# Optimization experiments

Hardware: AMD Instinct MI355X
Metric: run time of the kernel (lower is better)

## Reference

```python
import jax, jax.numpy as jnp
import numpy as np

N_LAYERS = 6
N_HEADS = 16
D_MODEL = 1024
D_HEAD = D_MODEL // N_HEADS
D_FF = 4096
VOCAB = 32000
MAX_LEN = 1024
B, T = 2, 1024
NEG = -1e9
EPS = 1e-5


def layernorm(x, s, b):
    mu = jnp.mean(x, axis=-1, keepdims=True)
    var = jnp.mean(jnp.square(x - mu), axis=-1, keepdims=True)
    return (x - mu) * jax.lax.rsqrt(var + EPS) * s + b


def setup_inputs() -> dict:
    key = jax.random.key(0)
    ks = jax.random.split(key, 8)
    s = 0.02
    return {
        "idx": jax.random.randint(ks[0], (B, T), 0, VOCAB),
        "tok_emb": jax.random.normal(ks[1], (VOCAB, D_MODEL), jnp.float32) * s,
        "pos_emb": jax.random.normal(ks[2], (MAX_LEN, D_MODEL), jnp.float32) * s,
        "ln1_s": jnp.ones((N_LAYERS, D_MODEL), jnp.float32),
        "ln1_b": jnp.zeros((N_LAYERS, D_MODEL), jnp.float32),
        "qkv_w": jax.random.normal(ks[3], (N_LAYERS, D_MODEL, 3 * D_MODEL), jnp.float32) * s,
        "qkv_b": jnp.zeros((N_LAYERS, 3 * D_MODEL), jnp.float32),
        "out_w": jax.random.normal(ks[4], (N_LAYERS, D_MODEL, D_MODEL), jnp.float32) * s,
        "out_b": jnp.zeros((N_LAYERS, D_MODEL), jnp.float32),
        "ln2_s": jnp.ones((N_LAYERS, D_MODEL), jnp.float32),
        "ln2_b": jnp.zeros((N_LAYERS, D_MODEL), jnp.float32),
        "mlp_w1": jax.random.normal(ks[5], (N_LAYERS, D_MODEL, D_FF), jnp.float32) * s,
        "mlp_b1": jnp.zeros((N_LAYERS, D_FF), jnp.float32),
        "mlp_w2": jax.random.normal(ks[6], (N_LAYERS, D_FF, D_MODEL), jnp.float32) * s,
        "mlp_b2": jnp.zeros((N_LAYERS, D_MODEL), jnp.float32),
        "lnf_s": jnp.ones((D_MODEL,), jnp.float32),
        "lnf_b": jnp.zeros((D_MODEL,), jnp.float32),
        "head_w": jax.random.normal(ks[7], (D_MODEL, VOCAB), jnp.float32) * s,
    }


def reference(idx, tok_emb, pos_emb, ln1_s, ln1_b, qkv_w, qkv_b, out_w, out_b,
              ln2_s, ln2_b, mlp_w1, mlp_b1, mlp_w2, mlp_b2, lnf_s, lnf_b, head_w):
    b, t = idx.shape
    x = tok_emb[idx] + pos_emb[:t]  # [B,T,D]
    causal = jnp.tril(jnp.ones((t, t), dtype=bool))
    scale = 1.0 / np.sqrt(D_HEAD)
    for l in range(N_LAYERS):
        h = layernorm(x, ln1_s[l], ln1_b[l])
        qkv = h @ qkv_w[l] + qkv_b[l]  # [B,T,3D]
        q, k, v = jnp.split(qkv, 3, axis=-1)
        q = q.reshape(b, t, N_HEADS, D_HEAD).transpose(0, 2, 1, 3)
        k = k.reshape(b, t, N_HEADS, D_HEAD).transpose(0, 2, 1, 3)
        v = v.reshape(b, t, N_HEADS, D_HEAD).transpose(0, 2, 1, 3)
        att = jnp.einsum('bhqd,bhkd->bhqk', q, k) * scale
        att = jnp.where(causal, att, NEG)
        att = jax.nn.softmax(att, axis=-1)
        y = jnp.einsum('bhqk,bhkd->bhqd', att, v)
        y = y.transpose(0, 2, 1, 3).reshape(b, t, D_MODEL)
        x = x + (y @ out_w[l] + out_b[l])
        h = layernorm(x, ln2_s[l], ln2_b[l])
        m = jax.nn.gelu(h @ mlp_w1[l] + mlp_b1[l], approximate=False) @ mlp_w2[l] + mlp_b2[l]
        x = x + m
    x = layernorm(x, lnf_s, lnf_b)
    logits = x @ head_w  # [B,T,V]
    return logits
```

## Files before the change

kernel.cpp:

```cpp
#include <hip/hip_runtime.h>


#define T_SEQ 1024
#define NTOK  2048
#define DM    1024
#define DFF   4096
#define NH    16
#define DH    64
#define NL    6
#define VOCAB 32000

typedef short sx8 __attribute__((ext_vector_type(8)));
typedef float fx4 __attribute__((ext_vector_type(4)));
typedef unsigned short usx4 __attribute__((ext_vector_type(4)));
typedef unsigned int   uix4 __attribute__((ext_vector_type(4)));

__device__ __forceinline__ unsigned short f2bf(float f) {
  union { float f; unsigned u; } c; c.f = f;
  unsigned r = c.u + 0x7FFFu + ((c.u >> 16) & 1u);
  return (unsigned short)(r >> 16);
}

__device__ __forceinline__ void gload_lds16(const unsigned short* g, unsigned short* l) {
  __builtin_amdgcn_global_load_lds(
      (const __attribute__((address_space(1))) unsigned int*)g,
      (__attribute__((address_space(3))) unsigned int*)l, 16, 0, 0);
}

__device__ __forceinline__ int xcd_swizzle(int orig, int nwg) {
  int q = nwg >> 3, r = nwg & 7;
  int xcd = orig & 7, idx = orig >> 3;
  int base = (xcd < r) ? xcd * (q + 1) : r * (q + 1) + (xcd - r) * q;
  return base + idx;
}

__global__ __launch_bounds__(256) void k_embed(const int* __restrict__ idx,
                                               const float* __restrict__ tok,
                                               const float* __restrict__ pos,
                                               float* __restrict__ x) {
  int token = blockIdx.x;
  int t = token & (T_SEQ - 1);
  int id = idx[token];
  int c = threadIdx.x * 4;
  float4 tv = *(const float4*)&tok[(size_t)id * DM + c];
  float4 pv = *(const float4*)&pos[(size_t)t * DM + c];
  float4 r;
  r.x = tv.x + pv.x; r.y = tv.y + pv.y; r.z = tv.z + pv.z; r.w = tv.w + pv.w;
  *(float4*)&x[(size_t)token * DM + c] = r;
}

__global__ __launch_bounds__(256) void k_ln(const float* __restrict__ x,
                                            const float* __restrict__ g,
                                            const float* __restrict__ b,
                                            unsigned short* __restrict__ h) {
  int row = blockIdx.x;
  int tid = threadIdx.x;
  float4 v = *(const float4*)&x[(size_t)row * DM + tid * 4];
  float s = v.x + v.y + v.z + v.w;
  float q = v.x * v.x + v.y * v.y + v.z * v.z + v.w * v.w;
  for (int off = 32; off > 0; off >>= 1) {
    s += __shfl_down(s, off);
    q += __shfl_down(q, off);
  }
  __shared__ float red[8];
  int wid = tid >> 6, lane = tid & 63;
  if (lane == 0) { red[wid] = s; red[4 + wid] = q; }
  __syncthreads();
  s = red[0] + red[1] + red[2] + red[3];
  q = red[4] + red[5] + red[6] + red[7];
  float mu = s * (1.0f / DM);
  float var = q * (1.0f / DM) - mu * mu;
  float rstd = rsqrtf(var + 1e-5f);
  float4 gg = *(const float4*)&g[tid * 4];
  float4 bb = *(const float4*)&b[tid * 4];
  usx4 o;
  o[0] = f2bf((v.x - mu) * rstd * gg.x + bb.x);
  o[1] = f2bf((v.y - mu) * rstd * gg.y + bb.y);
  o[2] = f2bf((v.z - mu) * rstd * gg.z + bb.z);
  o[3] = f2bf((v.w - mu) * rstd * gg.w + bb.w);
  *(usx4*)&h[(size_t)row * DM + tid * 4] = o;
}

__global__ __launch_bounds__(256) void k_reduce_ln(const float* __restrict__ part,
                                                   float* __restrict__ x,
                                                   const float* __restrict__ g,
                                                   const float* __restrict__ b,
                                                   unsigned short* __restrict__ h) {
  int row = blockIdx.x;
  int tid = threadIdx.x;
  int c = tid * 4;
  float4 v = *(const float4*)&x[(size_t)row * DM + c];
#pragma unroll
  for (int s4 = 0; s4 < 4; ++s4) {
    float4 p = *(const float4*)&part[((size_t)s4 * NTOK + row) * DM + c];
    v.x += p.x; v.y += p.y; v.z += p.z; v.w += p.w;
  }
  *(float4*)&x[(size_t)row * DM + c] = v;
  float s = v.x + v.y + v.z + v.w;
  float q = v.x * v.x + v.y * v.y + v.z * v.z + v.w * v.w;
  for (int off = 32; off > 0; off >>= 1) {
    s += __shfl_down(s, off);
    q += __shfl_down(q, off);
  }
  __shared__ float red[8];
  int wid = tid >> 6, lane = tid & 63;
  if (lane == 0) { red[wid] = s; red[4 + wid] = q; }
  __syncthreads();
  s = red[0] + red[1] + red[2] + red[3];
  q = red[4] + red[5] + red[6] + red[7];
  float mu = s * (1.0f / DM);
  float var = q * (1.0f / DM) - mu * mu;
  float rstd = rsqrtf(var + 1e-5f);
  float4 gg = *(const float4*)&g[c];
  float4 bb = *(const float4*)&b[c];
  usx4 o;
  o[0] = f2bf((v.x - mu) * rstd * gg.x + bb.x);
  o[1] = f2bf((v.y - mu) * rstd * gg.y + bb.y);
  o[2] = f2bf((v.z - mu) * rstd * gg.z + bb.z);
  o[3] = f2bf((v.w - mu) * rstd * gg.w + bb.w);
  *(usx4*)&h[(size_t)row * DM + c] = o;
}

__global__ __launch_bounds__(256) void k_wtrans(const float* __restrict__ W,
                                                unsigned short* __restrict__ WT,
                                                int K, int N) {
  __shared__ float t[64][68];
  int k0 = blockIdx.x * 64, n0 = blockIdx.y * 64;
  int tid = threadIdx.x;
#pragma unroll
  for (int i = 0; i < 4; ++i) {
    int chunk = i * 256 + tid;
    int r = chunk >> 4, c = (chunk & 15) << 2;
    float4 v = *(const float4*)&W[(size_t)(k0 + r) * N + n0 + c];
    t[r][c] = v.x; t[r][c + 1] = v.y; t[r][c + 2] = v.z; t[r][c + 3] = v.w;
  }
  __syncthreads();
#pragma unroll
  for (int i = 0; i < 4; ++i) {
    int chunk = i * 256 + tid;
    int n = chunk >> 4, c = (chunk & 15) << 2;
    usx4 o;
    o[0] = f2bf(t[c][n]);
    o[1] = f2bf(t[c + 1][n]);
    o[2] = f2bf(t[c + 2][n]);
    o[3] = f2bf(t[c + 3][n]);
    *(usx4*)&WT[(size_t)(n0 + n) * K + k0 + c] = o;
  }
}

template <int EPI>
__global__ __launch_bounds__(256) void k_gemm(const unsigned short* __restrict__ A,
                                              const unsigned short* __restrict__ BT,
                                              const float* __restrict__ bias,
                                              float* __restrict__ part,
                                              unsigned short* __restrict__ outb,
                                              float* __restrict__ outf,
                                              int N, int K, int NT, int KS) {
  __shared__ unsigned short As[128 * 64];
  __shared__ unsigned short Bs[128 * 64];
  int tid = threadIdx.x;
  int wid = tid >> 6, lane = tid & 63;
  int lr = lane & 15, lg = lane >> 4;

  int id = xcd_swizzle(blockIdx.x, gridDim.x);
  int mt = id & 15;
  int rest = id >> 4;
  int nt = rest % NT;
  int ks = rest / NT;
  int m0 = mt * 128, n0 = nt * 128;
  int Kslice = K / KS;
  int kbeg = ks * Kslice, kend = kbeg + Kslice;

  int wm = (wid >> 1) * 64, wn = (wid & 1) * 64;

  fx4 acc[4][4] = {};

  for (int kt = kbeg; kt < kend; kt += 64) {
    __syncthreads();
#pragma unroll
    for (int i = 0; i < 4; ++i) {
      int chunk = i * 256 + tid;
      int r = chunk >> 3;
      int slot = chunk & 7;
      int c = ((slot ^ (r & 7)) << 3);
      gload_lds16(&A[(size_t)(m0 + r) * K + kt + c], &As[chunk << 3]);
      gload_lds16(&BT[(size_t)(n0 + r) * K + kt + c], &Bs[chunk << 3]);
    }
    __syncthreads();
#pragma unroll
    for (int kk = 0; kk < 2; ++kk) {
      int slotz = (kk * 4 + lg) ^ (lr & 7);
      sx8 fa[4], fb[4];
#pragma unroll
      for (int mi = 0; mi < 4; ++mi)
        fa[mi] = *(const sx8*)&As[(wm + mi * 16 + lr) * 64 + slotz * 8];
#pragma unroll
      for (int ni = 0; ni < 4; ++ni)
        fb[ni] = *(const sx8*)&Bs[(wn + ni * 16 + lr) * 64 + slotz * 8];
#pragma unroll
      for (int mi = 0; mi < 4; ++mi)
#pragma unroll
        for (int ni = 0; ni < 4; ++ni)
          acc[mi][ni] = __builtin_amdgcn_mfma_f32_16x16x32_bf16(fb[ni], fa[mi], acc[mi][ni], 0, 0, 0);
    }
  }

#pragma unroll
  for (int ni = 0; ni < 4; ++ni) {
    int col0 = n0 + wn + ni * 16 + lg * 4;
    float4 bv = {0.f, 0.f, 0.f, 0.f};
    if (bias && ks == 0) bv = *(const float4*)&bias[col0];
#pragma unroll
    for (int mi = 0; mi < 4; ++mi) {
      int row = m0 + wm + mi * 16 + lr;
      float v0 = acc[mi][ni][0] + bv.x;
      float v1 = acc[mi][ni][1] + bv.y;
      float v2 = acc[mi][ni][2] + bv.z;
      float v3 = acc[mi][ni][3] + bv.w;
      if constexpr (EPI == 0) {
        int bb = row >> 10, tt = row & 1023;
        if (col0 < 2048) {
          int which = col0 >> 10;
          int hc = col0 & 1023;
          usx4 o = {f2bf(v0), f2bf(v1), f2bf(v2), f2bf(v3)};
          *(usx4*)&outb[(size_t)which * NTOK * DM +
                        (((size_t)bb * NH + (hc >> 6)) * T_SEQ + tt) * DH + (hc & 63)] = o;
        } else {
          int dc = col0 - 2048;
          unsigned short* vt = outb + (size_t)2 * NTOK * DM;
          size_t base = (((size_t)bb * NH + (dc >> 6)) * DH + (dc & 63)) * T_SEQ + tt;
          vt[base] = f2bf(v0);
          vt[base + T_SEQ] = f2bf(v1);
          vt[base + 2 * T_SEQ] = f2bf(v2);
          vt[base + 3 * T_SEQ] = f2bf(v3);
        }
      } else if constexpr (EPI == 1) {
        usx4 o;
        o[0] = f2bf(0.5f * v0 * (1.0f + erff(v0 * 0.70710678f)));
        o[1] = f2bf(0.5f * v1 * (1.0f + erff(v1 * 0.70710678f)));
        o[2] = f2bf(0.5f * v2 * (1.0f + erff(v2 * 0.70710678f)));
        o[3] = f2bf(0.5f * v3 * (1.0f + erff(v3 * 0.70710678f)));
        *(usx4*)&outb[(size_t)row * N + col0] = o;
      } else if constexpr (EPI == 2) {
        float4 o = {v0, v1, v2, v3};
        *(float4*)&part[((size_t)ks * NTOK + row) * DM + col0] = o;
      } else {
        float4 o = {v0, v1, v2, v3};
        *(float4*)&outf[(size_t)row * N + col0] = o;
      }
    }
  }
}

__global__ __launch_bounds__(256) void k_attn(const unsigned short* __restrict__ gq,
                                              const unsigned short* __restrict__ gk,
                                              const unsigned short* __restrict__ gvt,
                                              unsigned short* __restrict__ y) {
  __shared__ unsigned short Ks[128 * 64];
  __shared__ unsigned short Vt[64 * 128];
  __shared__ unsigned short Pw[4][16 * 136];
  int id = xcd_swizzle(blockIdx.x, gridDim.x);
  int bh = id >> 4, qt = 15 - (id & 15);
  int tid = threadIdx.x, wid = tid >> 6, lane = tid & 63;
  int lr = lane & 15, lg = lane >> 4;
  int q0 = qt * 64 + wid * 16;
  int qg = q0 + lr;

  sx8 qf[2];
  {
    const unsigned short* qp = gq + ((size_t)bh * T_SEQ + qg) * DH + lg * 8;
    qf[0] = *(const sx8*)qp;
    qf[1] = *(const sx8*)(qp + 32);
  }

  fx4 yacc[4] = {};
  float mrun = -1e30f, lrun = 0.f;

  int jmax = qt >> 1;
  for (int j = 0; j <= jmax; ++j) {
    int kt0 = j * 128;
    __syncthreads();
#pragma unroll
    for (int i = 0; i < 4; ++i) {
      int chunk = i * 256 + tid;
      {
        int r = chunk >> 3, s = chunk & 7;
        gload_lds16(&gk[((size_t)bh * T_SEQ + kt0 + r) * DH + ((s ^ (r & 7)) << 3)],
                    &Ks[chunk << 3]);
      }
      {
        int r = chunk >> 4, s = chunk & 15;
        gload_lds16(&gvt[((size_t)bh * DH + r) * T_SEQ + kt0 + ((s ^ (r & 15)) << 3)],
                    &Vt[chunk << 3]);
      }
    }
    __syncthreads();

    fx4 st[8] = {};
#pragma unroll
    for (int kk = 0; kk < 2; ++kk) {
      int slotz = (kk * 4 + lg) ^ (lr & 7);
#pragma unroll
      for (int mi = 0; mi < 8; ++mi) {
        sx8 kb = *(const sx8*)&Ks[(mi * 16 + lr) * 64 + slotz * 8];
        st[mi] = __builtin_amdgcn_mfma_f32_16x16x32_bf16(kb, qf[kk], st[mi], 0, 0, 0);
      }
    }

    float pvv[8][4];
    float pmax = -1e30f;
    bool lastj = (j == jmax);
#pragma unroll
    for (int mi = 0; mi < 8; ++mi)
#pragma unroll
      for (int rg = 0; rg < 4; ++rg) {
        float val = st[mi][rg] * 0.125f;
        if (lastj && (kt0 + mi * 16 + lg * 4 + rg) > qg) val = -1e30f;
        pvv[mi][rg] = val;
        pmax = fmaxf(pmax, val);
      }
    pmax = fmaxf(pmax, __shfl_xor(pmax, 16));
    pmax = fmaxf(pmax, __shfl_xor(pmax, 32));
    float mnew = fmaxf(mrun, pmax);
    float sc = __expf(mrun - mnew);
    mrun = mnew;
    float ps = 0.f;
#pragma unroll
    for (int mi = 0; mi < 8; ++mi)
#pragma unroll
      for (int rg = 0; rg < 4; ++rg) {
        float e = __expf(pvv[mi][rg] - mnew);
        pvv[mi][rg] = e;
        ps += e;
      }
    ps += __shfl_xor(ps, 16);
    ps += __shfl_xor(ps, 32);
    lrun = lrun * sc + ps;

#pragma unroll
    for (int dt = 0; dt < 4; ++dt)
#pragma unroll
      for (int rg = 0; rg < 4; ++rg) yacc[dt][rg] *= sc;

#pragma unroll
    for (int mi = 0; mi < 8; ++mi)
#pragma unroll
      for (int rp = 0; rp < 2; ++rp) {
        unsigned pk = (unsigned)f2bf(pvv[mi][rp * 2]) |
                      ((unsigned)f2bf(pvv[mi][rp * 2 + 1]) << 16);
        *(unsigned*)&Pw[wid][lr * 136 + mi * 16 + lg * 4 + rp * 2] = pk;
      }

#pragma unroll
    for (int kk = 0; kk < 4; ++kk) {
      sx8 pa = *(const sx8*)&Pw[wid][lr * 136 + kk * 32 + lg * 8];
      int slotz = (kk * 4 + lg) ^ lr;
#pragma unroll
      for (int dt = 0; dt < 4; ++dt) {
        sx8 vb = *(const sx8*)&Vt[(dt * 16 + lr) * 128 + slotz * 8];
        yacc[dt] = __builtin_amdgcn_mfma_f32_16x16x32_bf16(vb, pa, yacc[dt], 0, 0, 0);
      }
    }
  }

  float inv = 1.0f / lrun;
  int tok = (bh >> 4) * T_SEQ + qg;
  int colbase = (bh & 15) * DH;
#pragma unroll
  for (int dt = 0; dt < 4; ++dt) {
    usx4 o;
#pragma unroll
    for (int rg = 0; rg < 4; ++rg) o[rg] = f2bf(yacc[dt][rg] * inv);
    *(usx4*)&y[(size_t)tok * DM + colbase + dt * 16 + lg * 4] = o;
  }
}

extern "C" void kernel_launch(void* const* d_in, const int* in_sizes, int n_in,
                              void* d_out, int out_size, void* d_ws, size_t ws_size,
                              hipStream_t stream) {
  (void)in_sizes; (void)n_in; (void)out_size; (void)ws_size;
  const int*   idx     = (const int*)d_in[0];
  const float* tok_emb = (const float*)d_in[1];
  const float* pos_emb = (const float*)d_in[2];
  const float* ln1_s   = (const float*)d_in[3];
  const float* ln1_b   = (const float*)d_in[4];
  const float* qkv_w   = (const float*)d_in[5];
  const float* qkv_b   = (const float*)d_in[6];
  const float* out_w   = (const float*)d_in[7];
  const float* out_b   = (const float*)d_in[8];
  const float* ln2_s   = (const float*)d_in[9];
  const float* ln2_b   = (const float*)d_in[10];
  const float* mlp_w1  = (const float*)d_in[11];
  const float* mlp_b1  = (const float*)d_in[12];
  const float* mlp_w2  = (const float*)d_in[13];
  const float* mlp_b2  = (const float*)d_in[14];
  const float* lnf_s   = (const float*)d_in[15];
  const float* lnf_b   = (const float*)d_in[16];
  const float* head_w  = (const float*)d_in[17];

  char* p = (char*)d_ws;
  float* x          = (float*)p;          p += (size_t)NTOK * DM * 4;
  unsigned short* h = (unsigned short*)p; p += (size_t)NTOK * DM * 2;
  unsigned short* qkvb = (unsigned short*)p; p += (size_t)3 * NTOK * DM * 2;
  unsigned short* yb = (unsigned short*)p; p += (size_t)NTOK * DM * 2;
  unsigned short* m1 = (unsigned short*)p; p += (size_t)NTOK * DFF * 2;
  unsigned short* wt = (unsigned short*)p;
  float* part = (float*)(p + 32 * 1024 * 1024);

  dim3 blk(256);

  k_embed<<<NTOK, blk, 0, stream>>>(idx, tok_emb, pos_emb, x);
  k_ln<<<NTOK, blk, 0, stream>>>(x, ln1_s, ln1_b, h);

  for (int l = 0; l < NL; ++l) {
    k_wtrans<<<dim3(DM / 64, 3 * DM / 64), blk, 0, stream>>>(qkv_w + (size_t)l * DM * 3 * DM, wt, DM, 3 * DM);
    k_gemm<0><<<16 * 24, blk, 0, stream>>>(h, wt, qkv_b + l * 3 * DM,
                                           nullptr, qkvb, nullptr, 3 * DM, DM, 24, 1);
    k_attn<<<512, blk, 0, stream>>>(qkvb, qkvb + (size_t)NTOK * DM,
                                    qkvb + (size_t)2 * NTOK * DM, yb);
    k_wtrans<<<dim3(DM / 64, DM / 64), blk, 0, stream>>>(out_w + (size_t)l * DM * DM, wt, DM, DM);
    k_gemm<2><<<16 * 8 * 4, blk, 0, stream>>>(yb, wt, out_b + l * DM,
                                              part, nullptr, nullptr, DM, DM, 8, 4);
    k_reduce_ln<<<NTOK, blk, 0, stream>>>(part, x, ln2_s + l * DM, ln2_b + l * DM, h);
    k_wtrans<<<dim3(DM / 64, DFF / 64), blk, 0, stream>>>(mlp_w1 + (size_t)l * DM * DFF, wt, DM, DFF);
    k_gemm<1><<<16 * 32, blk, 0, stream>>>(h, wt, mlp_b1 + l * DFF,
                                           nullptr, m1, nullptr, DFF, DM, 32, 1);
    k_wtrans<<<dim3(DFF / 64, DM / 64), blk, 0, stream>>>(mlp_w2 + (size_t)l * DFF * DM, wt, DFF, DM);
    k_gemm<2><<<16 * 8 * 4, blk, 0, stream>>>(m1, wt, mlp_b2 + l * DM,
                                              part, nullptr, nullptr, DM, DFF, 8, 4);
    if (l < NL - 1)
      k_reduce_ln<<<NTOK, blk, 0, stream>>>(part, x, ln1_s + (l + 1) * DM, ln1_b + (l + 1) * DM, h);
    else
      k_reduce_ln<<<NTOK, blk, 0, stream>>>(part, x, lnf_s, lnf_b, h);
  }

  k_wtrans<<<dim3(DM / 64, VOCAB / 64), blk, 0, stream>>>(head_w, wt, DM, VOCAB);
  k_gemm<3><<<16 * 250, blk, 0, stream>>>(h, wt, nullptr,
                                          nullptr, nullptr, (float*)d_out, VOCAB, DM, 250, 1);
}
```

Before: 1.324 ms.

## Add 256x256 pipelined GEMM for LM head and lazy softmax rescale in attention

```diff
diff --git a/kernel.cpp b/kernel.cpp
--- a/kernel.cpp
+++ b/kernel.cpp
@@ -241,13 +241,127 @@
         o[2] = f2bf(0.5f * v2 * (1.0f + erff(v2 * 0.70710678f)));
         o[3] = f2bf(0.5f * v3 * (1.0f + erff(v3 * 0.70710678f)));
         *(usx4*)&outb[(size_t)row * N + col0] = o;
-      } else if constexpr (EPI == 2) {
+      } else {
         float4 o = {v0, v1, v2, v3};
         *(float4*)&part[((size_t)ks * NTOK + row) * DM + col0] = o;
-      } else {
-        float4 o = {v0, v1, v2, v3};
-        *(float4*)&outf[(size_t)row * N + col0] = o;
-      }
+      }
+    }
+  }
+}
+
+#define LDSUB(buf, ab, kk) (lds + (((buf) * 2 + (ab)) * 2 + (kk)) * 8192)
+
+__device__ __forceinline__ void stage_half(const unsigned short* g, int rowstride,
+                                           unsigned short* ldsbase, int tid, int k0) {
+#pragma unroll
+  for (int r = 0; r < 2; ++r) {
+    int chunk = r * 512 + tid;
+    int row = chunk >> 2, slot = chunk & 3;
+    gload_lds16(g + (size_t)row * rowstride + k0 + ((slot ^ (row & 3)) << 3),
+                ldsbase + (chunk << 3));
+  }
+}
+
+__global__ __launch_bounds__(512, 2) void k_gemm256(const unsigned short* __restrict__ A,
+                                                    const unsigned short* __restrict__ BT,
+                                                    float* __restrict__ outf,
+                                                    int N, int K) {
+  __shared__ unsigned short lds[8 * 8192];
+  int tid = threadIdx.x;
+  int wid = tid >> 6, lane = tid & 63;
+  int lr = lane & 15, lg = lane >> 4;
+  int wm2 = wid >> 2, wn4 = wid & 3;
+  int id = xcd_swizzle(blockIdx.x, gridDim.x);
+  int mt = id & 7, nt = id >> 3;
+  int m0 = mt * 256, n0 = nt * 256;
+  const unsigned short* Ab = A + (size_t)m0 * K;
+  const unsigned short* Bb = BT + (size_t)n0 * K;
+  int NIT = K >> 7;
+  int swz = (lg ^ (lr & 3)) << 3;
+
+  fx4 acc[8][4] = {};
+
+  stage_half(Ab, K, LDSUB(0, 0, 0), tid, 0);
+  stage_half(Bb, K, LDSUB(0, 1, 0), tid, 0);
+  stage_half(Ab, K, LDSUB(0, 0, 1), tid, 32);
+  stage_half(Bb, K, LDSUB(0, 1, 1), tid, 32);
+  stage_half(Ab, K, LDSUB(1, 0, 0), tid, 64);
+  stage_half(Bb, K, LDSUB(1, 1, 0), tid, 64);
+  stage_half(Ab, K, LDSUB(1, 0, 1), tid, 96);
+  asm volatile("s_waitcnt vmcnt(6)" ::: "memory");
+  __builtin_amdgcn_s_barrier();
+
+#define PHASE(BUF, KK, NH, LOADA, STG, VMW)                                          \
+  {                                                                                  \
+    if (LOADA) {                                                                     \
+      const unsigned short* sA = LDSUB(BUF, 0, KK);                                  \
+      _Pragma("unroll")                                                              \
+      for (int mi = 0; mi < 8; ++mi)                                                 \
+        fa[mi] = *(const sx8*)&sA[(wm2 * 128 + mi * 16 + lr) * 32 + swz];            \
+    }                                                                                \
+    {                                                                                \
+      const unsigned short* sB = LDSUB(BUF, 1, KK);                                  \
+      _Pragma("unroll")                                                              \
+      for (int j = 0; j < 2; ++j)                                                    \
+        fb[j] = *(const sx8*)&sB[(wn4 * 64 + (NH) * 32 + j * 16 + lr) * 32 + swz];   \
+    }                                                                                \
+    STG;                                                                             \
+    VMW;                                                                             \
+    __builtin_amdgcn_sched_barrier(0);                                               \
+    __builtin_amdgcn_s_barrier();                                                    \
+    asm volatile("s_waitcnt lgkmcnt(0)" ::: "memory");                               \
+    __builtin_amdgcn_sched_barrier(0);                                               \
+    __builtin_amdgcn_s_setprio(1);                                                   \
+    _Pragma("unroll")                                                                \
+    for (int mi = 0; mi < 8; ++mi) {                                                 \
+      acc[mi][(NH) * 2 + 0] = __builtin_amdgcn_mfma_f32_16x16x32_bf16(               \
+          fb[0], fa[mi], acc[mi][(NH) * 2 + 0], 0, 0, 0);                            \
+      acc[mi][(NH) * 2 + 1] = __builtin_amdgcn_mfma_f32_16x16x32_bf16(               \
+          fb[1], fa[mi], acc[mi][(NH) * 2 + 1], 0, 0, 0);                            \
+    }                                                                                \
+    __builtin_amdgcn_s_setprio(0);                                                   \
+    __builtin_amdgcn_sched_barrier(0);                                               \
+    __builtin_amdgcn_s_barrier();                                                    \
+  }
+
+  for (int it = 0; it < NIT; ++it) {
+    bool st = (it < NIT - 1);
+    bool last = (it == NIT - 1);
+    int t1k = (2 * it + 1) * 64;
+    int t2k = (2 * it + 2) * 64;
+    int t3k = (2 * it + 3) * 64;
+    sx8 fa[8], fb[2];
+
+    PHASE(0, 0, 0, true,
+          { stage_half(Bb, K, LDSUB(1, 1, 1), tid, t1k + 32); }, {});
+    PHASE(0, 0, 1, false,
+          { if (st) stage_half(Ab, K, LDSUB(0, 0, 0), tid, t2k); }, {});
+    PHASE(0, 1, 0, true,
+          { if (st) stage_half(Bb, K, LDSUB(0, 1, 0), tid, t2k); }, {});
+    PHASE(0, 1, 1, false,
+          { if (st) stage_half(Ab, K, LDSUB(0, 0, 1), tid, t2k + 32); },
+          { if (last) { asm volatile("s_waitcnt vmcnt(0)" ::: "memory"); }
+            else      { asm volatile("s_waitcnt vmcnt(6)" ::: "memory"); } });
+    PHASE(1, 0, 0, true,
+          { if (st) stage_half(Bb, K, LDSUB(0, 1, 1), tid, t2k + 32); }, {});
+    PHASE(1, 0, 1, false,
+          { if (st) stage_half(Ab, K, LDSUB(1, 0, 0), tid, t3k); }, {});
+    PHASE(1, 1, 0, true,
+          { if (st) stage_half(Bb, K, LDSUB(1, 1, 0), tid, t3k); }, {});
+    PHASE(1, 1, 1, false,
+          { if (st) stage_half(Ab, K, LDSUB(1, 0, 1), tid, t3k + 32); },
+          { if (!last) { asm volatile("s_waitcnt vmcnt(6)" ::: "memory"); } });
+  }
+#undef PHASE
+
+#pragma unroll
+  for (int mi = 0; mi < 8; ++mi) {
+    int row = m0 + wm2 * 128 + mi * 16 + lr;
+    float* orow = outf + (size_t)row * N + n0 + wn4 * 64 + lg * 4;
+#pragma unroll
+    for (int nj = 0; nj < 4; ++nj) {
+      float4 o = {acc[mi][nj][0], acc[mi][nj][1], acc[mi][nj][2], acc[mi][nj][3]};
+      *(float4*)&orow[nj * 16] = o;
     }
   }
 }
@@ -321,26 +435,28 @@
       }
     pmax = fmaxf(pmax, __shfl_xor(pmax, 16));
     pmax = fmaxf(pmax, __shfl_xor(pmax, 32));
-    float mnew = fmaxf(mrun, pmax);
-    float sc = __expf(mrun - mnew);
-    mrun = mnew;
+    if (!__all(pmax <= mrun + 8.0f)) {
+      float mnew = fmaxf(mrun, pmax);
+      float sc = __expf(mrun - mnew);
+      lrun *= sc;
+#pragma unroll
+      for (int dt = 0; dt < 4; ++dt)
+#pragma unroll
+        for (int rg = 0; rg < 4; ++rg) yacc[dt][rg] *= sc;
+      mrun = mnew;
+    }
     float ps = 0.f;
 #pragma unroll
     for (int mi = 0; mi < 8; ++mi)
 #pragma unroll
       for (int rg = 0; rg < 4; ++rg) {
-        float e = __expf(pvv[mi][rg] - mnew);
+        float e = __expf(pvv[mi][rg] - mrun);
         pvv[mi][rg] = e;
         ps += e;
       }
     ps += __shfl_xor(ps, 16);
     ps += __shfl_xor(ps, 32);
-    lrun = lrun * sc + ps;
-
-#pragma unroll
-    for (int dt = 0; dt < 4; ++dt)
-#pragma unroll
-      for (int rg = 0; rg < 4; ++rg) yacc[dt][rg] *= sc;
+    lrun += ps;
 
 #pragma unroll
     for (int mi = 0; mi < 8; ++mi)
@@ -435,6 +551,5 @@
   }
 
   k_wtrans<<<dim3(DM / 64, VOCAB / 64), blk, 0, stream>>>(head_w, wt, DM, VOCAB);
-  k_gemm<3><<<16 * 250, blk, 0, stream>>>(h, wt, nullptr,
-                                          nullptr, nullptr, (float*)d_out, VOCAB, DM, 250, 1);
-}
+  k_gemm256<<<1000, 512, 0, stream>>>(h, wt, (float*)d_out, VOCAB, DM);
+}
```

After: 1.217 ms. 1.09x faster.
